# Kernel tuning notes

Hardware: AMD Instinct MI355X
Metric: run time of the kernel (lower is better)

## Reference

```python
import jax, jax.numpy as jnp
import numpy as np

RADIUS = 3
DIAM = 2 * RADIUS + 1  # 7 -> 49 taps
KEY_DIM = 32
GN_GROUPS = 32
GN_EPS = 1e-5

_WE = [-0.03515625, 0.26171875, 0.87890625, -0.10546875]  # even outputs (frac 0.75)
_WO = [-0.10546875, 0.87890625, 0.26171875, -0.03515625]  # odd outputs (frac 0.25)


def _up2x_axis(x, axis):
    """2x bicubic upsample (a=-0.75, half-pixel, edge-clamped) along one axis."""
    pads = [(2, 2) if i == axis else (0, 0) for i in range(x.ndim)]
    xp = jnp.pad(x, pads, mode='edge')
    n = x.shape[axis]

    def sl(o):
        idx = [slice(None)] * x.ndim
        idx[axis] = slice(o, o + n)
        return xp[tuple(idx)]

    even = sum(_WE[j] * sl(j) for j in range(4))
    odd = sum(_WO[j] * sl(j + 1) for j in range(4))
    out = jnp.stack([even, odd], axis=axis + 1)
    shp = list(x.shape)
    shp[axis] = 2 * n
    return out.reshape(shp)


def bicubic_up2x(x):
    return _up2x_axis(_up2x_axis(x, 2), 3)


def conv1x1(x, w, b=None):
    # x: [B,C,H,W], w: [O,C]
    y = jnp.einsum('bchw,oc->bohw', x, w)
    if b is not None:
        y = y + b[None, :, None, None]
    return y


def jbu_step(source, guidance, rp_w1, rp_b1, rp_w2, rp_b2, temp, sigma):
    """One x2 JBULearnedRange step. source: [B,C,h,w], guidance: full-res [B,3,H0,W0]."""
    B, C, h, w = source.shape
    H, W = 2 * h, 2 * w
    g = jax.image.resize(guidance, (B, guidance.shape[1], H, W), method='linear')
    g = g.astype(source.dtype)

    # learned range projection (1x1 conv -> GELU -> 1x1 conv); dropout is eval identity
    proj = conv1x1(g, rp_w1, rp_b1)
    proj = jax.nn.gelu(proj, approximate=False)
    proj = conv1x1(proj, rp_w2, rp_b2)  # [B,K,H,W]

    pp = jnp.pad(proj, ((0, 0), (0, 0), (RADIUS, RADIUS), (RADIUS, RADIUS)), mode='reflect')
    # per-shift center<->neighbor similarity, shift order = row-major (dy outer, dx inner)
    sims = jnp.stack([jnp.sum(pp[:, :, dy:dy + H, dx:dx + W] * proj, axis=1)
                      for dy in range(DIAM) for dx in range(DIAM)], axis=1)  # [B,P,H,W]
    t = jnp.clip(jnp.exp(temp), 1e-4, 1e4)
    range_kernel = jax.nn.softmax(t * sims, axis=1)

    dist = jnp.linspace(-1.0, 1.0, DIAM)
    spatial = jnp.exp(-(dist[:, None] ** 2 + dist[None, :] ** 2) / (2.0 * sigma ** 2))
    spatial = spatial.reshape(1, DIAM * DIAM, 1, 1)

    ck = range_kernel * spatial
    ck = ck / jnp.clip(jnp.sum(ck, axis=1, keepdims=True), 1e-7, None)

    hr = bicubic_up2x(source)  # [B,C,H,W]
    hp = jnp.pad(hr, ((0, 0), (0, 0), (RADIUS, RADIUS), (RADIUS, RADIUS)), mode='reflect')
    out = jnp.zeros_like(hr)
    p = 0
    for dy in range(DIAM):
        for dx in range(DIAM):
            out = out + ck[:, p:p + 1] * hp[:, :, dy:dy + H, dx:dx + W]
            p += 1
    return out


def group_norm(x, w, b):
    B, C, H, W = x.shape
    xg = x.reshape(B, GN_GROUPS, C // GN_GROUPS, H, W)
    m = xg.mean(axis=(2, 3, 4), keepdims=True)
    v = jnp.mean((xg - m) ** 2, axis=(2, 3, 4), keepdims=True)
    xg = (xg - m) * jax.lax.rsqrt(v + GN_EPS)
    return xg.reshape(B, C, H, W) * w[None, :, None, None] + b[None, :, None, None]


def setup_inputs() -> dict:
    key = jax.random.key(0)
    ks = jax.random.split(key, 16)
    B, FD, MD, OD = 2, 384, 256, 256
    h, w = 48, 80
    inp = {
        'source': jax.random.normal(ks[0], (B, FD, h, w), dtype=jnp.float32),
        'guidance': jax.random.uniform(ks[1], (B, 3, 16 * h, 16 * w), dtype=jnp.float32),
        'pre_proj_w': jax.random.normal(ks[2], (MD, FD), dtype=jnp.float32) / np.sqrt(FD),
        'rp1_w1': jax.random.normal(ks[3], (KEY_DIM, 3), dtype=jnp.float32) / np.sqrt(3.0),
        'rp1_b1': jnp.zeros((KEY_DIM,), jnp.float32),
        'rp1_w2': jax.random.normal(ks[4], (KEY_DIM, KEY_DIM), dtype=jnp.float32) / np.sqrt(KEY_DIM),
        'rp1_b2': jnp.zeros((KEY_DIM,), jnp.float32),
        'temp1': jnp.asarray(0.0, jnp.float32),
        'sigma1': jnp.asarray(1.0, jnp.float32),
        'rp2_w1': jax.random.normal(ks[5], (KEY_DIM, 3), dtype=jnp.float32) / np.sqrt(3.0),
        'rp2_b1': jnp.zeros((KEY_DIM,), jnp.float32),
        'rp2_w2': jax.random.normal(ks[6], (KEY_DIM, KEY_DIM), dtype=jnp.float32) / np.sqrt(KEY_DIM),
        'rp2_b2': jnp.zeros((KEY_DIM,), jnp.float32),
        'temp2': jnp.asarray(0.0, jnp.float32),
        'sigma2': jnp.asarray(1.0, jnp.float32),
        'fixup_w': jax.random.normal(ks[7], (MD, MD), dtype=jnp.float32) / np.sqrt(MD),
        'gn_w': jnp.ones((MD,), jnp.float32),
        'gn_b': jnp.zeros((MD,), jnp.float32),
        'proj_w': jax.random.normal(ks[8], (OD, MD), dtype=jnp.float32) / np.sqrt(MD),
    }
    return inp


def reference(source, guidance, pre_proj_w,
              rp1_w1, rp1_b1, rp1_w2, rp1_b2, temp1, sigma1,
              rp2_w1, rp2_b1, rp2_w2, rp2_b2, temp2, sigma2,
              fixup_w, gn_w, gn_b, proj_w):
    x = conv1x1(source, pre_proj_w)
    x = jbu_step(x, guidance, rp1_w1, rp1_b1, rp1_w2, rp1_b2, temp1, sigma1)  # H/16 -> H/8
    x = jbu_step(x, guidance, rp2_w1, rp2_b1, rp2_w2, rp2_b2, temp2, sigma2)  # H/8 -> H/4
    x = x + 0.1 * conv1x1(x, fixup_w)  # FixUp residual (Dropout2d is eval identity)
    x = group_norm(x, gn_w, gn_b)
    return conv1x1(x, proj_w)
```

## Files before the change

kernel.cpp:

```cpp
#include <hip/hip_runtime.h>
#include <math.h>

#define B_ 2
#define C_ 256
#define FD_ 384
#define K_ 32
#define HW2 61440

typedef __attribute__((ext_vector_type(8))) short s8b;
typedef __attribute__((ext_vector_type(16))) float fvec16;
typedef __attribute__((ext_vector_type(4))) float f4;

__device__ __forceinline__ unsigned short f2bf(float f) {
    unsigned int u = __builtin_bit_cast(unsigned int, f);
    u = (u + 0x7fffu + ((u >> 16) & 1u)) >> 16;
    return (unsigned short)u;
}

__global__ void k_preproj(const float* __restrict__ src, const float* __restrict__ w,
                          float* __restrict__ out) {
    __shared__ float w_s[FD_];
    int bo = blockIdx.x;
    int b = bo >> 8, o = bo & 255;
    int tid = threadIdx.x;
    for (int i = tid; i < FD_; i += 256) w_s[i] = w[o * FD_ + i];
    __syncthreads();
    float acc[15];
#pragma unroll
    for (int k = 0; k < 15; k++) acc[k] = 0.f;
    const float* sp = src + (long)b * FD_ * 3840;
    for (int c = 0; c < FD_; c++) {
        float wv = w_s[c];
        const float* row = sp + (long)c * 3840;
#pragma unroll
        for (int k = 0; k < 15; k++) acc[k] += wv * row[tid + k * 256];
    }
    float* op = out + ((long)b * 256 + o) * 3840;
#pragma unroll
    for (int k = 0; k < 15; k++) op[tid + k * 256] = acc[k];
}

__global__ void k_down_h(const float* __restrict__ in, float* __restrict__ out, int Ho, float s) {
    long idx = (long)blockIdx.x * 256 + threadIdx.x;
    long total = (long)B_ * 3 * Ho * 1280;
    if (idx >= total) return;
    int x = (int)(idx % 1280);
    long t1 = idx / 1280;
    int i = (int)(t1 % Ho);
    long t2 = t1 / Ho;
    int c = (int)(t2 % 3);
    int b = (int)(t2 / 3);
    float sf = (i + 0.5f) * s - 0.5f;
    int j0 = (int)floorf(sf - s) + 1;
    int j1 = (int)ceilf(sf + s) - 1;
    float acc = 0.f, wsum = 0.f;
    const float* ip = in + ((long)(b * 3 + c) * 768) * 1280 + x;
    for (int j = j0; j <= j1; j++) {
        if (j < 0 || j >= 768) continue;
        float wv = 1.f - fabsf((float)j - sf) / s;
        acc += wv * ip[(long)j * 1280];
        wsum += wv;
    }
    out[idx] = acc / wsum;
}

__global__ void k_down_w(const float* __restrict__ in, float* __restrict__ out, int Ho, int Wo, float s) {
    long idx = (long)blockIdx.x * 256 + threadIdx.x;
    long total = (long)B_ * 3 * Ho * Wo;
    if (idx >= total) return;
    int i = (int)(idx % Wo);
    long t1 = idx / Wo;
    int y = (int)(t1 % Ho);
    long t2 = t1 / Ho;
    int c = (int)(t2 % 3);
    int b = (int)(t2 / 3);
    float sf = (i + 0.5f) * s - 0.5f;
    int j0 = (int)floorf(sf - s) + 1;
    int j1 = (int)ceilf(sf + s) - 1;
    float acc = 0.f, wsum = 0.f;
    const float* ip = in + ((long)(b * 3 + c) * Ho + y) * 1280;
    for (int j = j0; j <= j1; j++) {
        if (j < 0 || j >= 1280) continue;
        float wv = 1.f - fabsf((float)j - sf) / s;
        acc += wv * ip[j];
        wsum += wv;
    }
    out[idx] = acc / wsum;
}

__global__ void k_proj(const float* __restrict__ g, float* __restrict__ proj,
                       const float* __restrict__ w1, const float* __restrict__ b1,
                       const float* __restrict__ w2, const float* __restrict__ b2,
                       int HW) {
    __shared__ float w1_s[96], b1_s[32], w2_s[1024], b2_s[32];
    int tid = threadIdx.x;
    if (tid < 96) w1_s[tid] = w1[tid];
    if (tid < 32) { b1_s[tid] = b1[tid]; b2_s[tid] = b2[tid]; }
    for (int i = tid; i < 1024; i += 256) w2_s[i] = w2[i];
    __syncthreads();
    long idx = (long)blockIdx.x * 256 + tid;
    if (idx >= (long)B_ * HW) return;
    int b = (int)(idx / HW);
    int pix = (int)(idx % HW);
    const float* gp = g + (long)b * 3 * HW + pix;
    float g0 = gp[0], g1 = gp[HW], g2 = gp[2 * (long)HW];
    float hg[32];
#pragma unroll
    for (int k = 0; k < 32; k++) {
        float h = b1_s[k] + w1_s[k * 3] * g0 + w1_s[k * 3 + 1] * g1 + w1_s[k * 3 + 2] * g2;
        hg[k] = 0.5f * h * (1.f + erff(h * 0.70710678118654752f));
    }
    float* pp = proj + (long)b * 32 * HW + pix;
#pragma unroll
    for (int j = 0; j < 32; j++) {
        float a = b2_s[j];
#pragma unroll
        for (int k = 0; k < 32; k++) a += w2_s[j * 32 + k] * hg[k];
        pp[(long)j * HW] = a;
    }
}

__global__ __launch_bounds__(256) void k_ck(const float* __restrict__ proj,
                                            float* __restrict__ ckb,
                                            const float* __restrict__ temp,
                                            const float* __restrict__ sigma,
                                            int H, int W) {
    __shared__ __align__(16) float smem[9680];

    int tid = threadIdx.x;
    int tx = tid & 15, ty = tid >> 4;
    int x0 = blockIdx.x * 16, y0 = blockIdx.y * 16;
    int b = blockIdx.z;

    float ck[49];
#pragma unroll
    for (int p = 0; p < 49; p++) ck[p] = 0.f;

    const float* pb = proj + (long)b * 32 * H * W;
    const f4* hs4 = (const f4*)smem;
#pragma unroll 1
    for (int pass = 0; pass < 2; pass++) {
        int k0 = pass * 16;
        for (int i = tid; i < 16 * 484; i += 256) {
            int k = i / 484;
            int rem = i - k * 484;
            int yy = rem / 22, xx = rem - yy * 22;
            int y = y0 - 3 + yy; y = y < 0 ? -y : (y >= H ? 2 * H - 2 - y : y);
            int x = x0 - 3 + xx; x = x < 0 ? -x : (x >= W ? 2 * W - 2 - x : x);
            smem[rem * 20 + k] = pb[((long)(k0 + k) * H + y) * W + x];
        }
        __syncthreads();
        int pc = ((ty + 3) * 22 + (tx + 3)) * 5;
        f4 c0 = hs4[pc + 0], c1 = hs4[pc + 1], c2 = hs4[pc + 2], c3 = hs4[pc + 3];
#pragma unroll
        for (int dy = 0; dy < 7; dy++) {
#pragma unroll
            for (int dx = 0; dx < 7; dx++) {
                int pn = ((ty + dy) * 22 + (tx + dx)) * 5;
                f4 s = hs4[pn + 0] * c0;
                s += hs4[pn + 1] * c1;
                s += hs4[pn + 2] * c2;
                s += hs4[pn + 3] * c3;
                ck[dy * 7 + dx] += (s.x + s.y) + (s.z + s.w);
            }
        }
        __syncthreads();
    }

    {
        float t = expf(temp[0]);
        t = fminf(fmaxf(t, 1e-4f), 1e4f);
        float m = -1e30f;
#pragma unroll
        for (int p = 0; p < 49; p++) { ck[p] *= t; m = fmaxf(m, ck[p]); }
        float ssum = 0.f;
#pragma unroll
        for (int p = 0; p < 49; p++) { ck[p] = expf(ck[p] - m); ssum += ck[p]; }
        float inv = 1.f / ssum;
        float sg = sigma[0];
        float dc = 1.f / (2.f * sg * sg);
        float csum = 0.f;
#pragma unroll
        for (int p = 0; p < 49; p++) {
            int dy = p / 7, dx = p % 7;
            float d0 = (dy - 3) / 3.f, d1 = (dx - 3) / 3.f;
            float sp = expf(-(d0 * d0 + d1 * d1) * dc);
            ck[p] = ck[p] * inv * sp;
            csum += ck[p];
        }
        float r = 1.f / fmaxf(csum, 1e-7f);
#pragma unroll
        for (int p = 0; p < 49; p++) ck[p] *= r;
    }

    long HWl = (long)H * W;
    float* cp = ckb + (long)b * 49 * HWl + (long)(y0 + ty) * W + (x0 + tx);
#pragma unroll
    for (int p = 0; p < 49; p++) cp[(long)p * HWl] = ck[p];
}

template <int CS>
__global__ __launch_bounds__(256) void k_apply(const float* __restrict__ lo,
                                               const float* ckb,
                                               float* out,
                                               int H, int W, int h, int w) {
    __shared__ __align__(16) float smem[8952];

    int tid = threadIdx.x;
    int tx = tid & 15, ty = tid >> 4;
    int x0 = blockIdx.x * 16, y0 = blockIdx.y * 16;
    int b = blockIdx.z / CS;
    int c_base = (blockIdx.z % CS) * (256 / CS);

    long HWl = (long)H * W;
    const float* cp = ckb + (long)b * 49 * HWl + (long)(y0 + ty) * W + (x0 + tx);

    int ws_y = y0 - 3; if (ws_y < 0) ws_y = 0; if (ws_y > H - 22) ws_y = H - 22;
    int ws_x = x0 - 3; if (ws_x < 0) ws_x = 0; if (ws_x > W - 22) ws_x = W - 22;
    int ls_y = (ws_y >> 1) - 2, ls_x = (ws_x >> 1) - 2;
    int ry[7], rx[7];
#pragma unroll
    for (int d = 0; d < 7; d++) {
        int v = y0 + ty + d - 3; v = v < 0 ? -v : (v >= H ? 2 * H - 2 - v : v);
        ry[d] = v - ws_y;
        int u = x0 + tx + d - 3; u = u < 0 ? -u : (u >= W ? 2 * W - 2 - u : u);
        rx[d] = u - ws_x;
    }

    int lrow = ls_y + ty; lrow = lrow < 0 ? 0 : (lrow >= h ? h - 1 : lrow);
    int lcol = ls_x + tx; lcol = lcol < 0 ? 0 : (lcol >= w ? w - 1 : lcol);

    f4* lo4  = (f4*)smem;
    f4* tmp4 = (f4*)(smem + 2112);
    f4* hr4  = (f4*)(smem + 2112 + 2880);

    long hw = (long)h * w;

    const int nchunk = (256 / CS) / 8;
#pragma unroll 1
    for (int cc = 0; cc < nchunk; cc++) {
        int c0 = c_base + cc * 8;
        const float* lp = lo + (((long)b * 256 + c0) * h + lrow) * w + lcol;
        f4 va, vb;
        va.x = lp[0];      va.y = lp[hw];     va.z = lp[2 * hw]; va.w = lp[3 * hw];
        vb.x = lp[4 * hw]; vb.y = lp[5 * hw]; vb.z = lp[6 * hw]; vb.w = lp[7 * hw];
        lo4[ty * 33 + tx * 2 + 0] = va;
        lo4[ty * 33 + tx * 2 + 1] = vb;
        __syncthreads();

#pragma unroll
        for (int it = 0; it < 3; it++) {
            int e = tid + it * 256;
            if (e < 704) {
                int g = e & 1, rem = e >> 1;
                int j = rem / 22, Xp = rem - j * 22;
                int X = ws_x + Xp;
                int ix = (X >> 1) - ls_x;
                const f4* lr = lo4 + j * 33 + g;
                f4 v;
                if (X & 1)
                    v = -0.10546875f * lr[(ix - 1) * 2] + 0.87890625f * lr[ix * 2] + 0.26171875f * lr[(ix + 1) * 2] - 0.03515625f * lr[(ix + 2) * 2];
                else
                    v = -0.03515625f * lr[(ix - 2) * 2] + 0.26171875f * lr[(ix - 1) * 2] + 0.87890625f * lr[ix * 2] - 0.10546875f * lr[(ix + 1) * 2];
                tmp4[j * 45 + Xp * 2 + g] = v;
            }
        }
        __syncthreads();

#pragma unroll
        for (int it = 0; it < 4; it++) {
            int e = tid + it * 256;
            if (e < 968) {
                int g = e & 1, rem = e >> 1;
                int i = rem / 22, Xp = rem - i * 22;
                int Y = ws_y + i;
                int jy = (Y >> 1) - ls_y;
                const f4* tc = tmp4 + Xp * 2 + g;
                f4 v;
                if (Y & 1)
                    v = -0.10546875f * tc[(jy - 1) * 45] + 0.87890625f * tc[jy * 45] + 0.26171875f * tc[(jy + 1) * 45] - 0.03515625f * tc[(jy + 2) * 45];
                else
                    v = -0.03515625f * tc[(jy - 2) * 45] + 0.26171875f * tc[(jy - 1) * 45] + 0.87890625f * tc[jy * 45] - 0.10546875f * tc[(jy + 1) * 45];
                hr4[i * 45 + Xp * 2 + g] = v;
            }
        }
        __syncthreads();

        f4 acc0 = (f4)(0.f), acc1 = (f4)(0.f);
#pragma unroll
        for (int dy = 0; dy < 7; dy++) {
            float c_[7];
#pragma unroll
            for (int dx = 0; dx < 7; dx++) c_[dx] = cp[(long)(dy * 7 + dx) * HWl];
            const f4* hrow = hr4 + ry[dy] * 45;
#pragma unroll
            for (int dx = 0; dx < 7; dx++) {
                acc0 += c_[dx] * hrow[rx[dx] * 2];
                acc1 += c_[dx] * hrow[rx[dx] * 2 + 1];
            }
        }
        float* op = out + (((long)b * 256 + c0) * H + (y0 + ty)) * W + (x0 + tx);
        op[0]        = acc0.x;
        op[HWl]      = acc0.y;
        op[2 * HWl]  = acc0.z;
        op[3 * HWl]  = acc0.w;
        op[4 * HWl]  = acc1.x;
        op[5 * HWl]  = acc1.y;
        op[6 * HWl]  = acc1.z;
        op[7 * HWl]  = acc1.w;
    }
}

__global__ void k_prepw(const float* __restrict__ w, unsigned short* __restrict__ wf) {
    int blk = blockIdx.x;
    int lane = threadIdx.x;
    int mt = blk >> 4, ks = blk & 15;
    int o = mt * 32 + (lane & 31);
    int c = ks * 16 + (lane >> 5) * 8;
    const float* wp = w + (long)o * 256 + c;
    float4 v0 = *(const float4*)wp;
    float4 v1 = *(const float4*)(wp + 4);
    unsigned short* dst = wf + ((long)(blk * 64 + lane)) * 8;
    unsigned int r0 = f2bf(v0.x) | ((unsigned int)f2bf(v0.y) << 16);
    unsigned int r1 = f2bf(v0.z) | ((unsigned int)f2bf(v0.w) << 16);
    unsigned int r2 = f2bf(v1.x) | ((unsigned int)f2bf(v1.y) << 16);
    unsigned int r3 = f2bf(v1.z) | ((unsigned int)f2bf(v1.w) << 16);
    uint4 pk = {r0, r1, r2, r3};
    *(uint4*)dst = pk;
}

#define LDK 264
template <bool GN, bool RESID>
__global__ __launch_bounds__(256) void k_gemm256(float* __restrict__ x,
                                                 const unsigned short* __restrict__ wf,
                                                 const float* __restrict__ stats,
                                                 const float* __restrict__ gn_w,
                                                 const float* __restrict__ gn_b) {
    __shared__ unsigned short xs[64 * LDK];
    __shared__ float scl_s[256], sh_s[256];
    int tid = threadIdx.x;
    int b = blockIdx.y;
    int pix0 = blockIdx.x * 64;
    float* xb = x + (long)b * 256 * HW2;

    if (GN) {
        int c = tid;
        int g = c >> 3;
        float mean = stats[(b * 32 + g) * 2];
        float rstd = stats[(b * 32 + g) * 2 + 1];
        float s = rstd * gn_w[c];
        scl_s[c] = s;
        sh_s[c] = gn_b[c] - mean * s;
        __syncthreads();
    }

#pragma unroll
    for (int it = 0; it < 4; it++) {
        int c0 = ((tid >> 4) << 2) + it * 64;
        int px = (tid & 15) << 2;
        const float* gp = xb + (long)c0 * HW2 + pix0 + px;
        float4 v0 = *(const float4*)gp;
        float4 v1 = *(const float4*)(gp + HW2);
        float4 v2 = *(const float4*)(gp + 2 * HW2);
        float4 v3 = *(const float4*)(gp + 3 * HW2);
        if (GN) {
            float s0 = scl_s[c0], h0 = sh_s[c0];
            float s1 = scl_s[c0 + 1], h1 = sh_s[c0 + 1];
            float s2 = scl_s[c0 + 2], h2 = sh_s[c0 + 2];
            float s3 = scl_s[c0 + 3], h3 = sh_s[c0 + 3];
            v0.x = v0.x * s0 + h0; v0.y = v0.y * s0 + h0; v0.z = v0.z * s0 + h0; v0.w = v0.w * s0 + h0;
            v1.x = v1.x * s1 + h1; v1.y = v1.y * s1 + h1; v1.z = v1.z * s1 + h1; v1.w = v1.w * s1 + h1;
            v2.x = v2.x * s2 + h2; v2.y = v2.y * s2 + h2; v2.z = v2.z * s2 + h2; v2.w = v2.w * s2 + h2;
            v3.x = v3.x * s3 + h3; v3.y = v3.y * s3 + h3; v3.z = v3.z * s3 + h3; v3.w = v3.w * s3 + h3;
        }
        float p0[4] = {v0.x, v0.y, v0.z, v0.w};
        float p1[4] = {v1.x, v1.y, v1.z, v1.w};
        float p2[4] = {v2.x, v2.y, v2.z, v2.w};
        float p3[4] = {v3.x, v3.y, v3.z, v3.w};
#pragma unroll
        for (int p = 0; p < 4; p++) {
            ushort4 u;
            u.x = f2bf(p0[p]); u.y = f2bf(p1[p]); u.z = f2bf(p2[p]); u.w = f2bf(p3[p]);
            *(ushort4*)&xs[(px + p) * LDK + c0] = u;
        }
    }
    __syncthreads();

    int lane = tid & 63, wv = tid >> 6;
    fvec16 acc[2][2];
#pragma unroll
    for (int mi = 0; mi < 2; mi++)
#pragma unroll
        for (int ni = 0; ni < 2; ni++)
            acc[mi][ni] = (fvec16)(0.f);

    int n_in = lane & 31;
    int koff = (lane >> 5) * 8;
#pragma unroll
    for (int ks = 0; ks < 16; ks++) {
        s8b a0 = *(const s8b*)(wf + ((long)(((wv * 2 + 0) * 16 + ks) * 64 + lane)) * 8);
        s8b a1 = *(const s8b*)(wf + ((long)(((wv * 2 + 1) * 16 + ks) * 64 + lane)) * 8);
        s8b b0 = *(const s8b*)&xs[(0 + n_in) * LDK + ks * 16 + koff];
        s8b b1 = *(const s8b*)&xs[(32 + n_in) * LDK + ks * 16 + koff];
        acc[0][0] = __builtin_amdgcn_mfma_f32_32x32x16_bf16(a0, b0, acc[0][0], 0, 0, 0);
        acc[0][1] = __builtin_amdgcn_mfma_f32_32x32x16_bf16(a0, b1, acc[0][1], 0, 0, 0);
        acc[1][0] = __builtin_amdgcn_mfma_f32_32x32x16_bf16(a1, b0, acc[1][0], 0, 0, 0);
        acc[1][1] = __builtin_amdgcn_mfma_f32_32x32x16_bf16(a1, b1, acc[1][1], 0, 0, 0);
    }

    int hh = lane >> 5;
#pragma unroll
    for (int mi = 0; mi < 2; mi++) {
        int mt = wv * 2 + mi;
#pragma unroll
        for (int ni = 0; ni < 2; ni++) {
            int pix = pix0 + ni * 32 + n_in;
#pragma unroll
            for (int r = 0; r < 16; r++) {
                int row = (r & 3) + 8 * (r >> 2) + 4 * hh;
                long addr = (long)(mt * 32 + row) * HW2 + pix;
                if (RESID)
                    xb[addr] = xb[addr] + 0.1f * acc[mi][ni][r];
                else
                    xb[addr] = acc[mi][ni][r];
            }
        }
    }
}

__global__ void k_gnpart(const float* __restrict__ x, double* __restrict__ part) {
    __shared__ double s_s[256], q_s[256];
    int blk = blockIdx.x;
    int bg = blk >> 4, ch = blk & 15;
    const int CHUNK = 8 * HW2 / 16;
    const float* xp = x + (long)bg * 8 * HW2 + (long)ch * CHUNK;
    double s = 0.0, q = 0.0;
    for (int i = threadIdx.x; i < CHUNK; i += 256) {
        float v = xp[i];
        s += v; q += (double)v * v;
    }
    s_s[threadIdx.x] = s; q_s[threadIdx.x] = q;
    __syncthreads();
    for (int st = 128; st > 0; st >>= 1) {
        if (threadIdx.x < st) { s_s[threadIdx.x] += s_s[threadIdx.x + st]; q_s[threadIdx.x] += q_s[threadIdx.x + st]; }
        __syncthreads();
    }
    if (threadIdx.x == 0) {
        part[blk * 2] = s_s[0];
        part[blk * 2 + 1] = q_s[0];
    }
}

__global__ void k_gnred(const double* __restrict__ part, float* __restrict__ stats) {
    int bg = threadIdx.x;
    double s = 0.0, q = 0.0;
    for (int ch = 0; ch < 16; ch++) {
        s += part[(bg * 16 + ch) * 2];
        q += part[(bg * 16 + ch) * 2 + 1];
    }
    double N = 8.0 * HW2;
    double mean = s / N;
    double var = q / N - mean * mean;
    stats[bg * 2] = (float)mean;
    stats[bg * 2 + 1] = (float)(1.0 / sqrt(var + 1e-5));
}

extern "C" void kernel_launch(void* const* d_in, const int* in_sizes, int n_in,
                              void* d_out, int out_size, void* d_ws, size_t ws_size,
                              hipStream_t stream) {
    const float* src      = (const float*)d_in[0];
    const float* guidance = (const float*)d_in[1];
    const float* pre_w    = (const float*)d_in[2];
    const float* rp1_w1   = (const float*)d_in[3];
    const float* rp1_b1   = (const float*)d_in[4];
    const float* rp1_w2   = (const float*)d_in[5];
    const float* rp1_b2   = (const float*)d_in[6];
    const float* temp1    = (const float*)d_in[7];
    const float* sigma1   = (const float*)d_in[8];
    const float* rp2_w1   = (const float*)d_in[9];
    const float* rp2_b1   = (const float*)d_in[10];
    const float* rp2_w2   = (const float*)d_in[11];
    const float* rp2_b2   = (const float*)d_in[12];
    const float* temp2    = (const float*)d_in[13];
    const float* sigma2   = (const float*)d_in[14];
    const float* fixup_w  = (const float*)d_in[15];
    const float* gn_w     = (const float*)d_in[16];
    const float* gn_b     = (const float*)d_in[17];
    const float* proj_w   = (const float*)d_in[18];
    float* out = (float*)d_out;

    char* ws = (char*)d_ws;
    size_t off = 0;
    auto alloc = [&](size_t bytes) { size_t o = off; off = (off + bytes + 255) & ~(size_t)255; return o; };
    float* gdown  = (float*)(ws + alloc((size_t)2 * 3 * 192 * 1280 * 4));
    float* gbuf   = (float*)(ws + alloc((size_t)2 * 3 * 192 * 320 * 4));
    float* projb  = (float*)(ws + alloc((size_t)2 * 32 * 192 * 320 * 4));
    float* x1     = (float*)(ws + alloc((size_t)2 * 256 * 48 * 80 * 4));
    float* out1   = (float*)(ws + alloc((size_t)2 * 256 * 96 * 160 * 4));
    float* ckbuf  = (float*)(ws + alloc((size_t)2 * 49 * 192 * 320 * 4));
    unsigned short* wfFix  = (unsigned short*)(ws + alloc(65536 * 2));
    unsigned short* wfProj = (unsigned short*)(ws + alloc(65536 * 2));
    double* gpart = (double*)(ws + alloc(1024 * 2 * 8));
    float* stats  = (float*)(ws + alloc(64 * 2 * 4));

    k_prepw<<<128, 64, 0, stream>>>(fixup_w, wfFix);
    k_prepw<<<128, 64, 0, stream>>>(proj_w, wfProj);

    k_preproj<<<512, 256, 0, stream>>>(src, pre_w, x1);

    {
        const int H = 96, W = 160, HW = H * W;
        k_down_h<<<(2 * 3 * H * 1280) / 256, 256, 0, stream>>>(guidance, gdown, H, 8.f);
        k_down_w<<<(2 * 3 * HW + 255) / 256, 256, 0, stream>>>(gdown, gbuf, H, W, 8.f);
        k_proj<<<(2 * HW + 255) / 256, 256, 0, stream>>>(gbuf, projb, rp1_w1, rp1_b1, rp1_w2, rp1_b2, HW);
        k_ck<<<dim3(W / 16, H / 16, 2), 256, 0, stream>>>(projb, ckbuf, temp1, sigma1, H, W);
        k_apply<4><<<dim3(W / 16, H / 16, 2 * 4), 256, 0, stream>>>(x1, ckbuf, out1, H, W, 48, 80);
    }

    {
        const int H = 192, W = 320, HW = H * W;
        k_down_h<<<(2 * 3 * H * 1280) / 256, 256, 0, stream>>>(guidance, gdown, H, 4.f);
        k_down_w<<<(2 * 3 * HW + 255) / 256, 256, 0, stream>>>(gdown, gbuf, H, W, 4.f);
        k_proj<<<(2 * HW + 255) / 256, 256, 0, stream>>>(gbuf, projb, rp2_w1, rp2_b1, rp2_w2, rp2_b2, HW);
        k_ck<<<dim3(W / 16, H / 16, 2), 256, 0, stream>>>(projb, ckbuf, temp2, sigma2, H, W);
        k_apply<4><<<dim3(W / 16, H / 16, 2 * 4), 256, 0, stream>>>(out1, ckbuf, out, H, W, 96, 160);
    }

    k_gemm256<false, true><<<dim3(960, 2), 256, 0, stream>>>(out, wfFix, nullptr, nullptr, nullptr);
    k_gnpart<<<1024, 256, 0, stream>>>(out, gpart);
    k_gnred<<<1, 64, 0, stream>>>(gpart, stats);
    k_gemm256<true, false><<<dim3(960, 2), 256, 0, stream>>>(out, wfProj, stats, gn_w, gn_b);
}
```

Baseline: 920.4 us.

## Fuse GroupNorm statistics into residual GEMM, register-block preproj, tweak apply indexing

The FixUp residual GEMM now accumulates per-group sums and sums of squares in its epilogue, first through LDS atomics and then as per-block partials. This removes the separate k_gnpart pass that re-read the full activation tensor. A single-block reduction kernel then walks 960 partials for each of the 64 groups serially, and the partials are kept in float rather than double, which may cost some accuracy. k_preproj computes two output channels per block so each source load is reused twice, and k_apply gains an occupancy hint and precomputed scaled offsets.

```diff
diff --git a/kernel.cpp b/kernel.cpp
--- a/kernel.cpp
+++ b/kernel.cpp
@@ -19,25 +19,32 @@
 
 __global__ void k_preproj(const float* __restrict__ src, const float* __restrict__ w,
                           float* __restrict__ out) {
-    __shared__ float w_s[FD_];
+    __shared__ float w_s[2 * FD_];
     int bo = blockIdx.x;
-    int b = bo >> 8, o = bo & 255;
+    int b = bo >> 7, o = (bo & 127) * 2;
     int tid = threadIdx.x;
-    for (int i = tid; i < FD_; i += 256) w_s[i] = w[o * FD_ + i];
+    for (int i = tid; i < 2 * FD_; i += 256) w_s[i] = w[o * FD_ + i];
     __syncthreads();
-    float acc[15];
-#pragma unroll
-    for (int k = 0; k < 15; k++) acc[k] = 0.f;
+    float a0[15], a1[15];
+#pragma unroll
+    for (int k = 0; k < 15; k++) { a0[k] = 0.f; a1[k] = 0.f; }
     const float* sp = src + (long)b * FD_ * 3840;
     for (int c = 0; c < FD_; c++) {
-        float wv = w_s[c];
+        float wv0 = w_s[c];
+        float wv1 = w_s[FD_ + c];
         const float* row = sp + (long)c * 3840;
 #pragma unroll
-        for (int k = 0; k < 15; k++) acc[k] += wv * row[tid + k * 256];
+        for (int k = 0; k < 15; k++) {
+            float r = row[tid + k * 256];
+            a0[k] += wv0 * r;
+            a1[k] += wv1 * r;
+        }
     }
     float* op = out + ((long)b * 256 + o) * 3840;
 #pragma unroll
-    for (int k = 0; k < 15; k++) op[tid + k * 256] = acc[k];
+    for (int k = 0; k < 15; k++) op[tid + k * 256] = a0[k];
+#pragma unroll
+    for (int k = 0; k < 15; k++) op[3840 + tid + k * 256] = a1[k];
 }
 
 __global__ void k_down_h(const float* __restrict__ in, float* __restrict__ out, int Ho, float s) {
@@ -200,10 +207,10 @@
 }
 
 template <int CS>
-__global__ __launch_bounds__(256) void k_apply(const float* __restrict__ lo,
-                                               const float* ckb,
-                                               float* out,
-                                               int H, int W, int h, int w) {
+__global__ __launch_bounds__(256, 4) void k_apply(const float* __restrict__ lo,
+                                                  const float* ckb,
+                                                  float* out,
+                                                  int H, int W, int h, int w) {
     __shared__ __align__(16) float smem[8952];
 
     int tid = threadIdx.x;
@@ -222,9 +229,9 @@
 #pragma unroll
     for (int d = 0; d < 7; d++) {
         int v = y0 + ty + d - 3; v = v < 0 ? -v : (v >= H ? 2 * H - 2 - v : v);
-        ry[d] = v - ws_y;
+        ry[d] = (v - ws_y) * 45;
         int u = x0 + tx + d - 3; u = u < 0 ? -u : (u >= W ? 2 * W - 2 - u : u);
-        rx[d] = u - ws_x;
+        rx[d] = (u - ws_x) * 2;
     }
 
     int lrow = ls_y + ty; lrow = lrow < 0 ? 0 : (lrow >= h ? h - 1 : lrow);
@@ -292,11 +299,11 @@
             float c_[7];
 #pragma unroll
             for (int dx = 0; dx < 7; dx++) c_[dx] = cp[(long)(dy * 7 + dx) * HWl];
-            const f4* hrow = hr4 + ry[dy] * 45;
+            const f4* hrow = hr4 + ry[dy];
 #pragma unroll
             for (int dx = 0; dx < 7; dx++) {
-                acc0 += c_[dx] * hrow[rx[dx] * 2];
-                acc1 += c_[dx] * hrow[rx[dx] * 2 + 1];
+                acc0 += c_[dx] * hrow[rx[dx]];
+                acc1 += c_[dx] * hrow[rx[dx] + 1];
             }
         }
         float* op = out + (((long)b * 256 + c0) * H + (y0 + ty)) * W + (x0 + tx);
@@ -335,13 +342,17 @@
                                                  const unsigned short* __restrict__ wf,
                                                  const float* __restrict__ stats,
                                                  const float* __restrict__ gn_w,
-                                                 const float* __restrict__ gn_b) {
+                                                 const float* __restrict__ gn_b,
+                                                 float* __restrict__ part) {
     __shared__ unsigned short xs[64 * LDK];
     __shared__ float scl_s[256], sh_s[256];
+    __shared__ float gs[64];
     int tid = threadIdx.x;
     int b = blockIdx.y;
     int pix0 = blockIdx.x * 64;
     float* xb = x + (long)b * 256 * HW2;
+
+    if (RESID && tid < 64) gs[tid] = 0.f;
 
     if (GN) {
         int c = tid;
@@ -409,6 +420,13 @@
     }
 
     int hh = lane >> 5;
+    float ls[2][4], lq[2][4];
+    if (RESID) {
+#pragma unroll
+        for (int mi = 0; mi < 2; mi++)
+#pragma unroll
+            for (int gq = 0; gq < 4; gq++) { ls[mi][gq] = 0.f; lq[mi][gq] = 0.f; }
+    }
 #pragma unroll
     for (int mi = 0; mi < 2; mi++) {
         int mt = wv * 2 + mi;
@@ -419,50 +437,47 @@
             for (int r = 0; r < 16; r++) {
                 int row = (r & 3) + 8 * (r >> 2) + 4 * hh;
                 long addr = (long)(mt * 32 + row) * HW2 + pix;
-                if (RESID)
-                    xb[addr] = xb[addr] + 0.1f * acc[mi][ni][r];
-                else
+                if (RESID) {
+                    float v = xb[addr] + 0.1f * acc[mi][ni][r];
+                    xb[addr] = v;
+                    ls[mi][r >> 2] += v;
+                    lq[mi][r >> 2] += v * v;
+                } else {
                     xb[addr] = acc[mi][ni][r];
+                }
             }
         }
     }
-}
-
-__global__ void k_gnpart(const float* __restrict__ x, double* __restrict__ part) {
-    __shared__ double s_s[256], q_s[256];
-    int blk = blockIdx.x;
-    int bg = blk >> 4, ch = blk & 15;
-    const int CHUNK = 8 * HW2 / 16;
-    const float* xp = x + (long)bg * 8 * HW2 + (long)ch * CHUNK;
+    if (RESID) {
+#pragma unroll
+        for (int mi = 0; mi < 2; mi++)
+#pragma unroll
+            for (int gq = 0; gq < 4; gq++) {
+                int g = (wv * 2 + mi) * 4 + gq;
+                atomicAdd(&gs[g * 2], ls[mi][gq]);
+                atomicAdd(&gs[g * 2 + 1], lq[mi][gq]);
+            }
+        __syncthreads();
+        if (tid < 64) {
+            int g = tid >> 1, which = tid & 1;
+            part[((long)(b * 32 + g) * 960 + blockIdx.x) * 2 + which] = gs[tid];
+        }
+    }
+}
+
+__global__ void k_gnred2(const float* __restrict__ part, float* __restrict__ stats) {
+    int t = threadIdx.x;
+    const float* p = part + (long)t * 960 * 2;
     double s = 0.0, q = 0.0;
-    for (int i = threadIdx.x; i < CHUNK; i += 256) {
-        float v = xp[i];
-        s += v; q += (double)v * v;
-    }
-    s_s[threadIdx.x] = s; q_s[threadIdx.x] = q;
-    __syncthreads();
-    for (int st = 128; st > 0; st >>= 1) {
-        if (threadIdx.x < st) { s_s[threadIdx.x] += s_s[threadIdx.x + st]; q_s[threadIdx.x] += q_s[threadIdx.x + st]; }
-        __syncthreads();
-    }
-    if (threadIdx.x == 0) {
-        part[blk * 2] = s_s[0];
-        part[blk * 2 + 1] = q_s[0];
-    }
-}
-
-__global__ void k_gnred(const double* __restrict__ part, float* __restrict__ stats) {
-    int bg = threadIdx.x;
-    double s = 0.0, q = 0.0;
-    for (int ch = 0; ch < 16; ch++) {
-        s += part[(bg * 16 + ch) * 2];
-        q += part[(bg * 16 + ch) * 2 + 1];
+    for (int i = 0; i < 960; i++) {
+        s += p[2 * i];
+        q += p[2 * i + 1];
     }
     double N = 8.0 * HW2;
     double mean = s / N;
     double var = q / N - mean * mean;
-    stats[bg * 2] = (float)mean;
-    stats[bg * 2 + 1] = (float)(1.0 / sqrt(var + 1e-5));
+    stats[t * 2] = (float)mean;
+    stats[t * 2 + 1] = (float)(1.0 / sqrt(var + 1e-5));
 }
 
 extern "C" void kernel_launch(void* const* d_in, const int* in_sizes, int n_in,
@@ -500,13 +515,13 @@
     float* ckbuf  = (float*)(ws + alloc((size_t)2 * 49 * 192 * 320 * 4));
     unsigned short* wfFix  = (unsigned short*)(ws + alloc(65536 * 2));
     unsigned short* wfProj = (unsigned short*)(ws + alloc(65536 * 2));
-    double* gpart = (double*)(ws + alloc(1024 * 2 * 8));
+    float* gpart  = (float*)(ws + alloc((size_t)64 * 960 * 2 * 4));
     float* stats  = (float*)(ws + alloc(64 * 2 * 4));
 
     k_prepw<<<128, 64, 0, stream>>>(fixup_w, wfFix);
     k_prepw<<<128, 64, 0, stream>>>(proj_w, wfProj);
 
-    k_preproj<<<512, 256, 0, stream>>>(src, pre_w, x1);
+    k_preproj<<<256, 256, 0, stream>>>(src, pre_w, x1);
 
     {
         const int H = 96, W = 160, HW = H * W;
@@ -526,8 +541,7 @@
         k_apply<4><<<dim3(W / 16, H / 16, 2 * 4), 256, 0, stream>>>(out1, ckbuf, out, H, W, 96, 160);
     }
 
-    k_gemm256<false, true><<<dim3(960, 2), 256, 0, stream>>>(out, wfFix, nullptr, nullptr, nullptr);
-    k_gnpart<<<1024, 256, 0, stream>>>(out, gpart);
-    k_gnred<<<1, 64, 0, stream>>>(gpart, stats);
-    k_gemm256<true, false><<<dim3(960, 2), 256, 0, stream>>>(out, wfProj, stats, gn_w, gn_b);
-}
+    k_gemm256<false, true><<<dim3(960, 2), 256, 0, stream>>>(out, wfFix, nullptr, nullptr, nullptr, gpart);
+    k_gnred2<<<1, 64, 0, stream>>>(gpart, stats);
+    k_gemm256<true, false><<<dim3(960, 2), 256, 0, stream>>>(out, wfProj, stats, gn_w, gn_b, nullptr);
+}
```

After: 1.470 ms. +59.7%, slower.
